# Kernel optimization log

Hardware: AMD Instinct MI355X
Metric: run time of the kernel (lower is better)

The kernel has to match this reference:

```python
import jax, jax.numpy as jnp
import numpy as np

N_AGENTS = 8
S_DIM = 96
A_DIM = 32
ATT_DIM = 128   # attention_dim == hidden_dim of Attention
N_HEADS = 4
HEAD_DIM = ATT_DIM // N_HEADS
HIDDEN_1 = 128
SA_DIM = S_DIM + A_DIM  # 128, matches Attention in_dim
BATCH = 32768

leaky = lambda x: jax.nn.leaky_relu(x, negative_slope=0.01)


def setup_inputs() -> dict:
    key = jax.random.key(0)
    ks = jax.random.split(key, 18)
    sc = 0.05
    inp = {
        "s": jax.random.normal(ks[0], (BATCH, N_AGENTS * S_DIM), dtype=jnp.float32),
        "a": jax.random.uniform(ks[1], (BATCH, N_AGENTS * A_DIM), dtype=jnp.float32),
        # self agent (id=0) state encoder
        "W_enc_s": jax.random.normal(ks[2], (S_DIM, ATT_DIM), dtype=jnp.float32) * sc,
        "b_enc_s": jax.random.normal(ks[3], (ATT_DIM,), dtype=jnp.float32) * sc,
        # other agents' (1..7) distinct encoder_fc_sa weights, stacked
        "W_enc_sa": jax.random.normal(ks[4], (N_AGENTS - 1, SA_DIM, ATT_DIM), dtype=jnp.float32) * sc,
        "b_enc_sa": jax.random.normal(ks[5], (N_AGENTS - 1, ATT_DIM), dtype=jnp.float32) * sc,
        # attention block
        "Wq": jax.random.normal(ks[6], (ATT_DIM, ATT_DIM), dtype=jnp.float32) * sc,
        "Wk": jax.random.normal(ks[7], (ATT_DIM, ATT_DIM), dtype=jnp.float32) * sc,
        "Wv": jax.random.normal(ks[8], (ATT_DIM, ATT_DIM), dtype=jnp.float32) * sc,
        "bv": jax.random.normal(ks[9], (ATT_DIM,), dtype=jnp.float32) * sc,
        "Wo": jax.random.normal(ks[10], (ATT_DIM, ATT_DIM), dtype=jnp.float32) * sc,
        "bo": jax.random.normal(ks[11], (ATT_DIM,), dtype=jnp.float32) * sc,
        # head MLP
        "W_fc1": jax.random.normal(ks[12], (2 * ATT_DIM, HIDDEN_1), dtype=jnp.float32) * sc,
        "b_fc1": jax.random.normal(ks[13], (HIDDEN_1,), dtype=jnp.float32) * sc,
        "W_fc2": jax.random.normal(ks[14], (HIDDEN_1, A_DIM), dtype=jnp.float32) * sc,
        "b_fc2": jax.random.normal(ks[15], (A_DIM,), dtype=jnp.float32) * sc,
    }
    return inp


def reference(s, a, W_enc_s, b_enc_s, W_enc_sa, b_enc_sa,
              Wq, Wk, Wv, bv, Wo, bo, W_fc1, b_fc1, W_fc2, b_fc2):
    B = s.shape[0]
    n_other = N_AGENTS - 1

    # self agent (id=0) state encoding
    s_i_c = s[:, :S_DIM]                                   # [B, S]
    s_i = leaky(s_i_c @ W_enc_s + b_enc_s)                 # [B, D]

    # other agents' (state, action) slices -> per-agent linear + leakyrelu
    s_others = s[:, S_DIM:].reshape(B, n_other, S_DIM)     # [B, n, S]
    a_others = a[:, A_DIM:].reshape(B, n_other, A_DIM)     # [B, n, A]
    sa = jnp.concatenate([s_others, a_others], axis=-1)    # [B, n, S+A]
    e_k = leaky(jnp.einsum('bnf,nfd->bnd', sa, W_enc_sa) + b_enc_sa)  # [B, n, D]

    # multi-head attention: single query token (self), keys = other agents
    Q = (s_i @ Wq).reshape(B, N_HEADS, HEAD_DIM)                       # [B, H, d]
    K = jnp.einsum('bnd,de->bne', e_k, Wk).reshape(B, n_other, N_HEADS, HEAD_DIM)
    V = leaky(jnp.einsum('bnd,de->bne', e_k, Wv) + bv).reshape(B, n_other, N_HEADS, HEAD_DIM)
    scores = jnp.einsum('bhd,bnhd->bhn', Q, K) / np.sqrt(HEAD_DIM)     # [B, H, n]
    w = jax.nn.softmax(scores, axis=-1)
    attn = jnp.einsum('bhn,bnhd->bhd', w, V).reshape(B, ATT_DIM)       # [B, D]
    other_values = attn @ Wo + bo                                      # [B, D]

    # Q head
    X = jnp.concatenate([s_i, other_values], axis=1)       # [B, 2D]
    h = leaky(X @ W_fc1 + b_fc1)                           # [B, hidden_1]
    all_q = h @ W_fc2 + b_fc2                              # [B, A]

    int_acs = jnp.argmax(a[:, :A_DIM], axis=1, keepdims=True)   # [B, 1]
    q = jnp.take_along_axis(all_q, int_acs, axis=1)             # [B, 1]
    return (q, all_q)
```

## Files before the change

kernel.cpp:

```cpp
#include <hip/hip_runtime.h>
#include <math.h>


typedef __attribute__((ext_vector_type(8))) short bf16x8;
typedef __attribute__((ext_vector_type(4))) float f32x4;
typedef __attribute__((ext_vector_type(4))) __bf16 bf16x4f;

#define LROW 128
#define TRB 32

__device__ __forceinline__ float lrelu(float x){ return x > 0.f ? x : 0.01f * x; }

__device__ __forceinline__ unsigned short f2bf(float x){
    union { float f; unsigned u; } c; c.f = x;
    unsigned u = c.u; u += 0x7fffu + ((u >> 16) & 1u);
    return (unsigned short)(u >> 16);
}
__device__ __forceinline__ ushort4 pack4v(f32x4 v){
    union { bf16x4f b; ushort4 u; } c;
    c.b = __builtin_convertvector(v, bf16x4f);
    return c.u;
}
__device__ __forceinline__ f32x4 ldg_nt4(const float* p){
    return __builtin_nontemporal_load((const f32x4*)p);
}

__device__ __forceinline__ int sw(int row, int col){
    return row * LROW + (col ^ ((row & 7) << 3));
}

__device__ __forceinline__ bf16x8 ldA(const unsigned short* __restrict__ WT, int Kc,
                                      int m0, int kc, int lane){
    return *(const bf16x8*)(WT + ((((size_t)(m0 >> 4)) * Kc + kc) << 9) + lane * 8);
}
__device__ __forceinline__ bf16x8 ldB(const unsigned short* L, int n0, int kc, int lane){
    int row = n0 + (lane & 15);
    int col = kc * 32 + (lane >> 4) * 8;
    return *(const bf16x8*)(L + sw(row, col));
}
__device__ __forceinline__ void stB(unsigned short* L, int row, int col, ushort4 v){
    *(ushort4*)(L + sw(row, col)) = v;
}

template<int NKC>
__device__ __forceinline__ void ldW(const unsigned short* __restrict__ WT, int Kc, int M0,
                                    int kc0, int lane, bf16x8 F[2][NKC]){
#pragma unroll
    for (int mt = 0; mt < 2; ++mt)
#pragma unroll
        for (int kc = 0; kc < NKC; ++kc)
            F[mt][kc] = ldA(WT, Kc, M0 + mt * 16, kc0 + kc, lane);
}

template<int NKC>
__device__ __forceinline__ void mmR(const bf16x8 F[2][NKC], const unsigned short* Ls,
                                    int lane, f32x4 acc[2][2]){
#pragma unroll
    for (int kc = 0; kc < NKC; ++kc) {
        bf16x8 b[2];
#pragma unroll
        for (int nt = 0; nt < 2; ++nt) b[nt] = ldB(Ls, nt * 16, kc, lane);
#pragma unroll
        for (int mt = 0; mt < 2; ++mt)
#pragma unroll
            for (int nt = 0; nt < 2; ++nt)
                acc[mt][nt] = __builtin_amdgcn_mfma_f32_16x16x32_bf16(F[mt][kc], b[nt], acc[mt][nt], 0, 0, 0);
    }
}

template<int NKC>
__device__ __forceinline__ void mmG(const unsigned short* __restrict__ WT, int Kc, int M0,
                                    int kc0, const unsigned short* Ls, int lane,
                                    f32x4 acc[2][2]){
    bf16x8 F[2][NKC];
    ldW<NKC>(WT, Kc, M0, kc0, lane, F);
    mmR<NKC>(F, Ls, lane, acc);
}

__device__ __forceinline__ void ld_sa_f(const float* __restrict__ s, const float* __restrict__ a,
                                        int row0, int n, int t, f32x4 sf[3], f32x4& af){
#pragma unroll
    for (int i = 0; i < 3; ++i) {
        int idx = t + 256 * i; int r = idx / 24, c4 = idx % 24;
        sf[i] = ldg_nt4(s + (size_t)(row0 + r) * 768 + 96 + 96 * n + c4 * 4);
    }
    af = ldg_nt4(a + (size_t)(row0 + (t >> 3)) * 256 + 32 + 32 * n + (t & 7) * 4);
}
__device__ __forceinline__ void st_sa(unsigned short* buf, int t,
                                      const f32x4 sf[3], const f32x4 af){
#pragma unroll
    for (int i = 0; i < 3; ++i) {
        int idx = t + 256 * i; int r = idx / 24, c4 = idx % 24;
        stB(buf, r, c4 * 4, pack4v(sf[i]));
    }
    stB(buf, t >> 3, 96 + (t & 7) * 4, pack4v(af));
}

__device__ __forceinline__ int froff(int q, int f, int Kc){
    return (((q >> 4) * Kc + (f >> 5)) << 9) + (((f >> 3) & 3) << 7) + ((q & 15) << 3) + (f & 7);
}

__global__ void wprep(const float* __restrict__ Ws, const float* __restrict__ Wsa,
                      const float* __restrict__ Wq_, const float* __restrict__ Wk_,
                      const float* __restrict__ Wv_, const float* __restrict__ Wo_,
                      const float* __restrict__ W1, const float* __restrict__ W2,
                      unsigned short* __restrict__ o)
{
    int id = blockIdx.x * 256 + threadIdx.x;
    if (id >= 229376) return;
    float v; int dst;
    if (id < 12288)        { int q = id / 96, f = id - q * 96;
                             v = Ws[f * 128 + q];              dst = froff(q, f, 3); }
    else if (id < 126976)  { int li = id - 12288; int n = li >> 14; int r = li & 16383;
                             int q = r >> 7, f = r & 127;
                             v = Wsa[n * 16384 + f * 128 + q]; dst = 12288 + n * 16384 + froff(q, f, 4); }
    else if (id < 143360)  { int li = id - 126976; int q = li >> 7, f = li & 127;
                             v = Wq_[f * 128 + q];             dst = 126976 + froff(q, f, 4); }
    else if (id < 159744)  { int li = id - 143360; int q = li >> 7, f = li & 127;
                             v = Wk_[f * 128 + q];             dst = 143360 + froff(q, f, 4); }
    else if (id < 176128)  { int li = id - 159744; int q = li >> 7, f = li & 127;
                             v = Wv_[f * 128 + q];             dst = 159744 + froff(q, f, 4); }
    else if (id < 192512)  { int li = id - 176128; int q = li >> 7, f = li & 127;
                             v = Wo_[f * 128 + q];             dst = 176128 + froff(q, f, 4); }
    else if (id < 225280)  { int li = id - 192512; int q = li >> 8, f = li & 255;
                             v = W1[f * 128 + q];              dst = 192512 + froff(q, f, 8); }
    else                   { int li = id - 225280; int q = li >> 7, f = li & 127;
                             v = W2[f * 32 + q];               dst = 225280 + froff(q, f, 4); }
    o[dst] = f2bf(v);
}

__global__ void __launch_bounds__(256, 2)
ac_mfma(const float* __restrict__ s, const float* __restrict__ a,
        const unsigned short* __restrict__ WS,
        const float* __restrict__ b_enc_s, const float* __restrict__ b_enc_sa,
        const float* __restrict__ bv, const float* __restrict__ bo,
        const float* __restrict__ b_fc1, const float* __restrict__ b_fc2,
        float* __restrict__ out_q, float* __restrict__ out_allq)
{
    __shared__ __align__(16) unsigned short SMEM[5 * TRB * LROW];
    unsigned short* bufA0 = SMEM;
    unsigned short* bufA1 = SMEM + TRB * LROW;
    unsigned short* sE0   = SMEM + 2 * TRB * LROW;
    unsigned short* sE1   = SMEM + 3 * TRB * LROW;
    unsigned short* sENC  = SMEM + 4 * TRB * LROW;

    const int t = threadIdx.x, lane = t & 63, wid = t >> 6;
    const int l15 = lane & 15, l4 = lane >> 4;
    const int M0 = 32 * wid;
    const int row0 = blockIdx.x * TRB;
    const float rsd = 0.17677669529663687f;

    const unsigned short* WencST = WS;
    const unsigned short* WsaT   = WS + 12288;
    const unsigned short* WqT    = WS + 126976;
    const unsigned short* WkT    = WS + 143360;
    const unsigned short* WvT    = WS + 159744;
    const unsigned short* WoT    = WS + 176128;
    const unsigned short* W1T    = WS + 192512;
    const unsigned short* W2T    = WS + 225280;

    f32x4 sf[3]; f32x4 af;

    ld_sa_f(s, a, row0, -1, t, sf, af);
    st_sa(bufA0, t, sf, af);
    __syncthreads();

    f32x4 acc[2][2];
#pragma unroll
    for (int mt = 0; mt < 2; ++mt)
#pragma unroll
        for (int nt = 0; nt < 2; ++nt) acc[mt][nt] = (f32x4){0.f, 0.f, 0.f, 0.f};
    mmG<3>(WencST, 3, M0, 0, bufA0, lane, acc);
    ld_sa_f(s, a, row0, 0, t, sf, af);
    __syncthreads();
#pragma unroll
    for (int mt = 0; mt < 2; ++mt) {
        float4 bb = *(const float4*)(b_enc_s + M0 + mt * 16 + l4 * 4);
#pragma unroll
        for (int nt = 0; nt < 2; ++nt) {
            f32x4 v;
            v[0] = lrelu(acc[mt][nt][0] + bb.x); v[1] = lrelu(acc[mt][nt][1] + bb.y);
            v[2] = lrelu(acc[mt][nt][2] + bb.z); v[3] = lrelu(acc[mt][nt][3] + bb.w);
            stB(sENC, nt * 16 + l15, M0 + mt * 16 + l4 * 4, pack4v(v));
        }
    }
    st_sa(bufA1, t, sf, af);
    __syncthreads();

    f32x4 q[2][2];
#pragma unroll
    for (int mt = 0; mt < 2; ++mt)
#pragma unroll
        for (int nt = 0; nt < 2; ++nt) q[mt][nt] = (f32x4){0.f, 0.f, 0.f, 0.f};
    mmG<4>(WqT, 4, M0, 0, sENC, lane, q);

    float4 bvf[2];
#pragma unroll
    for (int mt = 0; mt < 2; ++mt) bvf[mt] = *(const float4*)(bv + M0 + mt * 16 + l4 * 4);

    f32x4 atn[2][2];
#pragma unroll
    for (int mt = 0; mt < 2; ++mt)
#pragma unroll
        for (int nt = 0; nt < 2; ++nt) atn[mt][nt] = (f32x4){0.f, 0.f, 0.f, 0.f};
    float m_[2] = {-INFINITY, -INFINITY}, l_[2] = {0.f, 0.f};

    auto kv_phase = [&](const unsigned short* EB){
        f32x4 kk[2][2], vv[2][2];
#pragma unroll
        for (int mt = 0; mt < 2; ++mt)
#pragma unroll
            for (int nt = 0; nt < 2; ++nt) {
                kk[mt][nt] = (f32x4){0.f, 0.f, 0.f, 0.f};
                vv[mt][nt] = (f32x4){0.f, 0.f, 0.f, 0.f};
            }
#pragma unroll
        for (int kc = 0; kc < 4; ++kc) {
            bf16x8 b[2];
#pragma unroll
            for (int nt = 0; nt < 2; ++nt) b[nt] = ldB(EB, nt * 16, kc, lane);
#pragma unroll
            for (int mt = 0; mt < 2; ++mt) {
                bf16x8 fk = ldA(WkT, 4, M0 + mt * 16, kc, lane);
                bf16x8 fv = ldA(WvT, 4, M0 + mt * 16, kc, lane);
#pragma unroll
                for (int nt = 0; nt < 2; ++nt) {
                    kk[mt][nt] = __builtin_amdgcn_mfma_f32_16x16x32_bf16(fk, b[nt], kk[mt][nt], 0, 0, 0);
                    vv[mt][nt] = __builtin_amdgcn_mfma_f32_16x16x32_bf16(fv, b[nt], vv[mt][nt], 0, 0, 0);
                }
            }
        }
        float pr[2], corr[2];
#pragma unroll
        for (int nt = 0; nt < 2; ++nt) {
            float p = 0.f;
#pragma unroll
            for (int mt = 0; mt < 2; ++mt)
#pragma unroll
                for (int r = 0; r < 4; ++r) p = fmaf(q[mt][nt][r], kk[mt][nt][r], p);
            p += __shfl_xor(p, 16);
            p += __shfl_xor(p, 32);
            float sc = p * rsd;
            float mo = m_[nt], mn = fmaxf(mo, sc);
            pr[nt]   = __expf(sc - mn);
            corr[nt] = __expf(mo - mn);
            l_[nt] = l_[nt] * corr[nt] + pr[nt];
            m_[nt] = mn;
        }
#pragma unroll
        for (int mt = 0; mt < 2; ++mt)
#pragma unroll
            for (int nt = 0; nt < 2; ++nt)
#pragma unroll
                for (int r = 0; r < 4; ++r) {
                    float vx = lrelu(vv[mt][nt][r] + ((const float*)&bvf[mt])[r]);
                    atn[mt][nt][r] = fmaf(atn[mt][nt][r], corr[nt], pr[nt] * vx);
                }
    };

    for (int n = 0; n < 7; ++n) {
        unsigned short* stageRd = (n & 1) ? bufA0 : bufA1;
        unsigned short* stageWr = (n & 1) ? bufA1 : bufA0;
        unsigned short* eWr     = (n & 1) ? sE1 : sE0;
        unsigned short* eRd     = (n & 1) ? sE0 : sE1;

        if (n < 6) ld_sa_f(s, a, row0, n + 1, t, sf, af);
        bf16x8 F[2][4];
        ldW<4>(WsaT + n * 16384, 4, M0, 0, lane, F);

        if (n) kv_phase(eRd);

        f32x4 e[2][2];
#pragma unroll
        for (int mt = 0; mt < 2; ++mt)
#pragma unroll
            for (int nt = 0; nt < 2; ++nt) e[mt][nt] = (f32x4){0.f, 0.f, 0.f, 0.f};
        mmR<4>(F, stageRd, lane, e);

#pragma unroll
        for (int mt = 0; mt < 2; ++mt) {
            float4 bb = *(const float4*)(b_enc_sa + n * 128 + M0 + mt * 16 + l4 * 4);
#pragma unroll
            for (int nt = 0; nt < 2; ++nt) {
                f32x4 v;
                v[0] = lrelu(e[mt][nt][0] + bb.x); v[1] = lrelu(e[mt][nt][1] + bb.y);
                v[2] = lrelu(e[mt][nt][2] + bb.z); v[3] = lrelu(e[mt][nt][3] + bb.w);
                stB(eWr, nt * 16 + l15, M0 + mt * 16 + l4 * 4, pack4v(v));
            }
        }
        if (n < 6) st_sa(stageWr, t, sf, af);
        __syncthreads();
    }
    kv_phase(sE0);

#pragma unroll
    for (int mt = 0; mt < 2; ++mt)
#pragma unroll
        for (int nt = 0; nt < 2; ++nt) {
            float inv = 1.f / l_[nt];
            f32x4 v;
            v[0] = atn[mt][nt][0] * inv; v[1] = atn[mt][nt][1] * inv;
            v[2] = atn[mt][nt][2] * inv; v[3] = atn[mt][nt][3] * inv;
            stB(bufA0, nt * 16 + l15, M0 + mt * 16 + l4 * 4, pack4v(v));
        }
    __syncthreads();

#pragma unroll
    for (int mt = 0; mt < 2; ++mt)
#pragma unroll
        for (int nt = 0; nt < 2; ++nt) acc[mt][nt] = (f32x4){0.f, 0.f, 0.f, 0.f};
    mmG<4>(WoT, 4, M0, 0, bufA0, lane, acc);
#pragma unroll
    for (int mt = 0; mt < 2; ++mt) {
        float4 bb = *(const float4*)(bo + M0 + mt * 16 + l4 * 4);
#pragma unroll
        for (int nt = 0; nt < 2; ++nt) {
            f32x4 v;
            v[0] = acc[mt][nt][0] + bb.x; v[1] = acc[mt][nt][1] + bb.y;
            v[2] = acc[mt][nt][2] + bb.z; v[3] = acc[mt][nt][3] + bb.w;
            stB(sE0, nt * 16 + l15, M0 + mt * 16 + l4 * 4, pack4v(v));
        }
    }
    __syncthreads();

#pragma unroll
    for (int mt = 0; mt < 2; ++mt)
#pragma unroll
        for (int nt = 0; nt < 2; ++nt) acc[mt][nt] = (f32x4){0.f, 0.f, 0.f, 0.f};
    mmG<4>(W1T, 8, M0, 0, sENC, lane, acc);
    mmG<4>(W1T, 8, M0, 4, sE0, lane, acc);
#pragma unroll
    for (int mt = 0; mt < 2; ++mt) {
        float4 bb = *(const float4*)(b_fc1 + M0 + mt * 16 + l4 * 4);
#pragma unroll
        for (int nt = 0; nt < 2; ++nt) {
            f32x4 v;
            v[0] = lrelu(acc[mt][nt][0] + bb.x); v[1] = lrelu(acc[mt][nt][1] + bb.y);
            v[2] = lrelu(acc[mt][nt][2] + bb.z); v[3] = lrelu(acc[mt][nt][3] + bb.w);
            stB(bufA0, nt * 16 + l15, M0 + mt * 16 + l4 * 4, pack4v(v));
        }
    }
    __syncthreads();

    float* P = (float*)(SMEM + TRB * LROW);
    {
        bf16x8 a0 = ldA(W2T, 4, 0, wid, lane);
        bf16x8 a1 = ldA(W2T, 4, 16, wid, lane);
        bf16x8 b0 = ldB(bufA0, 0, wid, lane);
        bf16x8 b1 = ldB(bufA0, 16, wid, lane);
        f32x4 z = (f32x4){0.f, 0.f, 0.f, 0.f};
        f32x4 c00 = __builtin_amdgcn_mfma_f32_16x16x32_bf16(a0, b0, z, 0, 0, 0);
        f32x4 c01 = __builtin_amdgcn_mfma_f32_16x16x32_bf16(a0, b1, z, 0, 0, 0);
        f32x4 c10 = __builtin_amdgcn_mfma_f32_16x16x32_bf16(a1, b0, z, 0, 0, 0);
        f32x4 c11 = __builtin_amdgcn_mfma_f32_16x16x32_bf16(a1, b1, z, 0, 0, 0);
        *(f32x4*)(P + wid * 1024 + (l15     ) * 32 +      l4 * 4) = c00;
        *(f32x4*)(P + wid * 1024 + (16 + l15) * 32 +      l4 * 4) = c01;
        *(f32x4*)(P + wid * 1024 + (l15     ) * 32 + 16 + l4 * 4) = c10;
        *(f32x4*)(P + wid * 1024 + (16 + l15) * 32 + 16 + l4 * 4) = c11;
    }
    __syncthreads();

    float* S = (float*)sENC;
#pragma unroll
    for (int j = 0; j < 4; ++j) {
        int o = t + 256 * j; int row = o >> 5, f = o & 31;
        float v = P[row * 32 + f] + P[1024 + row * 32 + f]
                + P[2048 + row * 32 + f] + P[3072 + row * 32 + f] + b_fc2[f];
        out_allq[(size_t)(row0 + row) * 32 + f] = v;
        S[row * 33 + f] = v;
    }
    __syncthreads();

    if (t < TRB) {
        int row = row0 + t;
        float best = -INFINITY; int bi = 0;
#pragma unroll
        for (int jj = 0; jj < 8; ++jj) {
            f32x4 v = ldg_nt4(a + (size_t)row * 256 + jj * 4);
#pragma unroll
            for (int e2 = 0; e2 < 4; ++e2)
                if (v[e2] > best) { best = v[e2]; bi = jj * 4 + e2; }
        }
        out_q[row] = S[t * 33 + bi];
    }
}

extern "C" void kernel_launch(void* const* d_in, const int* in_sizes, int n_in,
                              void* d_out, int out_size, void* d_ws, size_t ws_size,
                              hipStream_t stream)
{
    (void)n_in; (void)out_size; (void)ws_size;
    const float* s        = (const float*)d_in[0];
    const float* a        = (const float*)d_in[1];
    const float* W_enc_s  = (const float*)d_in[2];
    const float* b_enc_s  = (const float*)d_in[3];
    const float* W_enc_sa = (const float*)d_in[4];
    const float* b_enc_sa = (const float*)d_in[5];
    const float* Wq       = (const float*)d_in[6];
    const float* Wk       = (const float*)d_in[7];
    const float* Wv       = (const float*)d_in[8];
    const float* bv       = (const float*)d_in[9];
    const float* Wo       = (const float*)d_in[10];
    const float* bo       = (const float*)d_in[11];
    const float* W_fc1    = (const float*)d_in[12];
    const float* b_fc1    = (const float*)d_in[13];
    const float* W_fc2    = (const float*)d_in[14];
    const float* b_fc2    = (const float*)d_in[15];

    int B = in_sizes[0] / 768;
    float* out_q    = (float*)d_out;
    float* out_allq = out_q + B;
    unsigned short* WS = (unsigned short*)d_ws;

    wprep<<<dim3(896), dim3(256), 0, stream>>>(W_enc_s, W_enc_sa, Wq, Wk, Wv, Wo,
                                               W_fc1, W_fc2, WS);
    ac_mfma<<<dim3(B / TRB), dim3(256), 0, stream>>>(s, a, WS, b_enc_s, b_enc_sa,
                                                     bv, bo, b_fc1, b_fc2,
                                                     out_q, out_allq);
}
```

Measured before the change: 66.63 us.

## Load input B-fragments directly from global into registers, drop LDS staging

Result: slower. 108.8 us (+63.3%).

```diff
diff --git a/kernel.cpp b/kernel.cpp
--- a/kernel.cpp
+++ b/kernel.cpp
@@ -4,7 +4,9 @@
 
 typedef __attribute__((ext_vector_type(8))) short bf16x8;
 typedef __attribute__((ext_vector_type(4))) float f32x4;
+typedef __attribute__((ext_vector_type(8))) float f32x8;
 typedef __attribute__((ext_vector_type(4))) __bf16 bf16x4f;
+typedef __attribute__((ext_vector_type(8))) __bf16 bf16x8f;
 
 #define LROW 128
 #define TRB 32
@@ -25,6 +27,17 @@
     return __builtin_nontemporal_load((const f32x4*)p);
 }
 
+__device__ __forceinline__ bf16x8 ldBg(const float* p){
+    f32x4 lo = *(const f32x4*)p;
+    f32x4 hi = *(const f32x4*)(p + 4);
+    f32x8 w;
+    w[0]=lo[0]; w[1]=lo[1]; w[2]=lo[2]; w[3]=lo[3];
+    w[4]=hi[0]; w[5]=hi[1]; w[6]=hi[2]; w[7]=hi[3];
+    union { bf16x8f b; bf16x8 s; } c;
+    c.b = __builtin_convertvector(w, bf16x8f);
+    return c.s;
+}
+
 __device__ __forceinline__ int sw(int row, int col){
     return row * LROW + (col ^ ((row & 7) << 3));
 }
@@ -43,57 +56,22 @@
 }
 
 template<int NKC>
-__device__ __forceinline__ void ldW(const unsigned short* __restrict__ WT, int Kc, int M0,
-                                    int kc0, int lane, bf16x8 F[2][NKC]){
-#pragma unroll
-    for (int mt = 0; mt < 2; ++mt)
-#pragma unroll
-        for (int kc = 0; kc < NKC; ++kc)
-            F[mt][kc] = ldA(WT, Kc, M0 + mt * 16, kc0 + kc, lane);
-}
-
-template<int NKC>
-__device__ __forceinline__ void mmR(const bf16x8 F[2][NKC], const unsigned short* Ls,
-                                    int lane, f32x4 acc[2][2]){
-#pragma unroll
-    for (int kc = 0; kc < NKC; ++kc) {
-        bf16x8 b[2];
-#pragma unroll
-        for (int nt = 0; nt < 2; ++nt) b[nt] = ldB(Ls, nt * 16, kc, lane);
-#pragma unroll
-        for (int mt = 0; mt < 2; ++mt)
-#pragma unroll
-            for (int nt = 0; nt < 2; ++nt)
-                acc[mt][nt] = __builtin_amdgcn_mfma_f32_16x16x32_bf16(F[mt][kc], b[nt], acc[mt][nt], 0, 0, 0);
-    }
-}
-
-template<int NKC>
 __device__ __forceinline__ void mmG(const unsigned short* __restrict__ WT, int Kc, int M0,
                                     int kc0, const unsigned short* Ls, int lane,
                                     f32x4 acc[2][2]){
-    bf16x8 F[2][NKC];
-    ldW<NKC>(WT, Kc, M0, kc0, lane, F);
-    mmR<NKC>(F, Ls, lane, acc);
-}
-
-__device__ __forceinline__ void ld_sa_f(const float* __restrict__ s, const float* __restrict__ a,
-                                        int row0, int n, int t, f32x4 sf[3], f32x4& af){
-#pragma unroll
-    for (int i = 0; i < 3; ++i) {
-        int idx = t + 256 * i; int r = idx / 24, c4 = idx % 24;
-        sf[i] = ldg_nt4(s + (size_t)(row0 + r) * 768 + 96 + 96 * n + c4 * 4);
-    }
-    af = ldg_nt4(a + (size_t)(row0 + (t >> 3)) * 256 + 32 + 32 * n + (t & 7) * 4);
-}
-__device__ __forceinline__ void st_sa(unsigned short* buf, int t,
-                                      const f32x4 sf[3], const f32x4 af){
-#pragma unroll
-    for (int i = 0; i < 3; ++i) {
-        int idx = t + 256 * i; int r = idx / 24, c4 = idx % 24;
-        stB(buf, r, c4 * 4, pack4v(sf[i]));
-    }
-    stB(buf, t >> 3, 96 + (t & 7) * 4, pack4v(af));
+#pragma unroll
+    for (int kc = 0; kc < NKC; ++kc) {
+        bf16x8 b[2];
+#pragma unroll
+        for (int nt = 0; nt < 2; ++nt) b[nt] = ldB(Ls, nt * 16, kc, lane);
+        bf16x8 f0 = ldA(WT, Kc, M0,      kc0 + kc, lane);
+        bf16x8 f1 = ldA(WT, Kc, M0 + 16, kc0 + kc, lane);
+#pragma unroll
+        for (int nt = 0; nt < 2; ++nt) {
+            acc[0][nt] = __builtin_amdgcn_mfma_f32_16x16x32_bf16(f0, b[nt], acc[0][nt], 0, 0, 0);
+            acc[1][nt] = __builtin_amdgcn_mfma_f32_16x16x32_bf16(f1, b[nt], acc[1][nt], 0, 0, 0);
+        }
+    }
 }
 
 __device__ __forceinline__ int froff(int q, int f, int Kc){
@@ -137,12 +115,11 @@
         const float* __restrict__ b_fc1, const float* __restrict__ b_fc2,
         float* __restrict__ out_q, float* __restrict__ out_allq)
 {
-    __shared__ __align__(16) unsigned short SMEM[5 * TRB * LROW];
-    unsigned short* bufA0 = SMEM;
-    unsigned short* bufA1 = SMEM + TRB * LROW;
-    unsigned short* sE0   = SMEM + 2 * TRB * LROW;
-    unsigned short* sE1   = SMEM + 3 * TRB * LROW;
-    unsigned short* sENC  = SMEM + 4 * TRB * LROW;
+    __shared__ __align__(16) unsigned short SMEM[4 * TRB * LROW];
+    unsigned short* sAux = SMEM;
+    unsigned short* sENC = SMEM + TRB * LROW;
+    unsigned short* sE0  = SMEM + 2 * TRB * LROW;
+    unsigned short* sE1  = SMEM + 3 * TRB * LROW;
 
     const int t = threadIdx.x, lane = t & 63, wid = t >> 6;
     const int l15 = lane & 15, l4 = lane >> 4;
@@ -159,20 +136,32 @@
     const unsigned short* W1T    = WS + 192512;
     const unsigned short* W2T    = WS + 225280;
 
-    f32x4 sf[3]; f32x4 af;
-
-    ld_sa_f(s, a, row0, -1, t, sf, af);
-    st_sa(bufA0, t, sf, af);
-    __syncthreads();
+    const float* srow[2]; const float* arow[2];
+#pragma unroll
+    for (int nt = 0; nt < 2; ++nt) {
+        int row = row0 + nt * 16 + l15;
+        srow[nt] = s + (size_t)row * 768;
+        arow[nt] = a + (size_t)row * 256;
+    }
 
     f32x4 acc[2][2];
 #pragma unroll
     for (int mt = 0; mt < 2; ++mt)
 #pragma unroll
         for (int nt = 0; nt < 2; ++nt) acc[mt][nt] = (f32x4){0.f, 0.f, 0.f, 0.f};
-    mmG<3>(WencST, 3, M0, 0, bufA0, lane, acc);
-    ld_sa_f(s, a, row0, 0, t, sf, af);
-    __syncthreads();
+#pragma unroll
+    for (int kc = 0; kc < 3; ++kc) {
+        bf16x8 b[2];
+#pragma unroll
+        for (int nt = 0; nt < 2; ++nt) b[nt] = ldBg(srow[nt] + kc * 32 + l4 * 8);
+        bf16x8 f0 = ldA(WencST, 3, M0,      kc, lane);
+        bf16x8 f1 = ldA(WencST, 3, M0 + 16, kc, lane);
+#pragma unroll
+        for (int nt = 0; nt < 2; ++nt) {
+            acc[0][nt] = __builtin_amdgcn_mfma_f32_16x16x32_bf16(f0, b[nt], acc[0][nt], 0, 0, 0);
+            acc[1][nt] = __builtin_amdgcn_mfma_f32_16x16x32_bf16(f1, b[nt], acc[1][nt], 0, 0, 0);
+        }
+    }
 #pragma unroll
     for (int mt = 0; mt < 2; ++mt) {
         float4 bb = *(const float4*)(b_enc_s + M0 + mt * 16 + l4 * 4);
@@ -184,7 +173,6 @@
             stB(sENC, nt * 16 + l15, M0 + mt * 16 + l4 * 4, pack4v(v));
         }
     }
-    st_sa(bufA1, t, sf, af);
     __syncthreads();
 
     f32x4 q[2][2];
@@ -259,14 +247,17 @@
     };
 
     for (int n = 0; n < 7; ++n) {
-        unsigned short* stageRd = (n & 1) ? bufA0 : bufA1;
-        unsigned short* stageWr = (n & 1) ? bufA1 : bufA0;
-        unsigned short* eWr     = (n & 1) ? sE1 : sE0;
-        unsigned short* eRd     = (n & 1) ? sE0 : sE1;
-
-        if (n < 6) ld_sa_f(s, a, row0, n + 1, t, sf, af);
-        bf16x8 F[2][4];
-        ldW<4>(WsaT + n * 16384, 4, M0, 0, lane, F);
+        unsigned short* eWr = (n & 1) ? sE1 : sE0;
+        unsigned short* eRd = (n & 1) ? sE0 : sE1;
+
+        bf16x8 bsa[2][4];
+#pragma unroll
+        for (int nt = 0; nt < 2; ++nt) {
+            const float* sb = srow[nt] + 96 + 96 * n;
+#pragma unroll
+            for (int kc = 0; kc < 3; ++kc) bsa[nt][kc] = ldBg(sb + kc * 32 + l4 * 8);
+            bsa[nt][3] = ldBg(arow[nt] + 32 + 32 * n + l4 * 8);
+        }
 
         if (n) kv_phase(eRd);
 
@@ -275,7 +266,16 @@
         for (int mt = 0; mt < 2; ++mt)
 #pragma unroll
             for (int nt = 0; nt < 2; ++nt) e[mt][nt] = (f32x4){0.f, 0.f, 0.f, 0.f};
-        mmR<4>(F, stageRd, lane, e);
+#pragma unroll
+        for (int kc = 0; kc < 4; ++kc) {
+            bf16x8 f0 = ldA(WsaT + n * 16384, 4, M0,      kc, lane);
+            bf16x8 f1 = ldA(WsaT + n * 16384, 4, M0 + 16, kc, lane);
+#pragma unroll
+            for (int nt = 0; nt < 2; ++nt) {
+                e[0][nt] = __builtin_amdgcn_mfma_f32_16x16x32_bf16(f0, bsa[nt][kc], e[0][nt], 0, 0, 0);
+                e[1][nt] = __builtin_amdgcn_mfma_f32_16x16x32_bf16(f1, bsa[nt][kc], e[1][nt], 0, 0, 0);
+            }
+        }
 
 #pragma unroll
         for (int mt = 0; mt < 2; ++mt) {
@@ -288,7 +288,6 @@
                 stB(eWr, nt * 16 + l15, M0 + mt * 16 + l4 * 4, pack4v(v));
             }
         }
-        if (n < 6) st_sa(stageWr, t, sf, af);
         __syncthreads();
     }
     kv_phase(sE0);
@@ -301,7 +300,7 @@
             f32x4 v;
             v[0] = atn[mt][nt][0] * inv; v[1] = atn[mt][nt][1] * inv;
             v[2] = atn[mt][nt][2] * inv; v[3] = atn[mt][nt][3] * inv;
-            stB(bufA0, nt * 16 + l15, M0 + mt * 16 + l4 * 4, pack4v(v));
+            stB(sAux, nt * 16 + l15, M0 + mt * 16 + l4 * 4, pack4v(v));
         }
     __syncthreads();
 
@@ -309,7 +308,7 @@
     for (int mt = 0; mt < 2; ++mt)
 #pragma unroll
         for (int nt = 0; nt < 2; ++nt) acc[mt][nt] = (f32x4){0.f, 0.f, 0.f, 0.f};
-    mmG<4>(WoT, 4, M0, 0, bufA0, lane, acc);
+    mmG<4>(WoT, 4, M0, 0, sAux, lane, acc);
 #pragma unroll
     for (int mt = 0; mt < 2; ++mt) {
         float4 bb = *(const float4*)(bo + M0 + mt * 16 + l4 * 4);
@@ -337,17 +336,17 @@
             f32x4 v;
             v[0] = lrelu(acc[mt][nt][0] + bb.x); v[1] = lrelu(acc[mt][nt][1] + bb.y);
             v[2] = lrelu(acc[mt][nt][2] + bb.z); v[3] = lrelu(acc[mt][nt][3] + bb.w);
-            stB(bufA0, nt * 16 + l15, M0 + mt * 16 + l4 * 4, pack4v(v));
-        }
-    }
-    __syncthreads();
-
-    float* P = (float*)(SMEM + TRB * LROW);
+            stB(sAux, nt * 16 + l15, M0 + mt * 16 + l4 * 4, pack4v(v));
+        }
+    }
+    __syncthreads();
+
+    float* P = (float*)(SMEM + 2 * TRB * LROW);
     {
         bf16x8 a0 = ldA(W2T, 4, 0, wid, lane);
         bf16x8 a1 = ldA(W2T, 4, 16, wid, lane);
-        bf16x8 b0 = ldB(bufA0, 0, wid, lane);
-        bf16x8 b1 = ldB(bufA0, 16, wid, lane);
+        bf16x8 b0 = ldB(sAux, 0, wid, lane);
+        bf16x8 b1 = ldB(sAux, 16, wid, lane);
         f32x4 z = (f32x4){0.f, 0.f, 0.f, 0.f};
         f32x4 c00 = __builtin_amdgcn_mfma_f32_16x16x32_bf16(a0, b0, z, 0, 0, 0);
         f32x4 c01 = __builtin_amdgcn_mfma_f32_16x16x32_bf16(a0, b1, z, 0, 0, 0);
@@ -360,7 +359,7 @@
     }
     __syncthreads();
 
-    float* S = (float*)sENC;
+    float* S = (float*)(SMEM + TRB * LROW);
 #pragma unroll
     for (int j = 0; j < 4; ++j) {
         int o = t + 256 * j; int row = o >> 5, f = o & 31;
```
